# Performance work log

Hardware: AMD Instinct MI355X
Metric: run time of the kernel (lower is better)

## Reference

```python
import jax, jax.numpy as jnp
import numpy as np

N_NODES = 100000
N_EDGES = 600000
IN_DIM = 128
OUT_DIM = 64


def setup_inputs() -> dict:
    key = jax.random.key(0)
    k1, k2, k3, k4, k5 = jax.random.split(key, 5)
    x = jax.random.normal(k1, (N_NODES, IN_DIM), dtype=jnp.float32)
    edge_index = jax.random.randint(k2, (2, N_EDGES), 0, N_NODES, dtype=jnp.int64)
    edge_weight = jax.random.uniform(k3, (N_EDGES,), dtype=jnp.float32)
    W1 = jax.random.normal(k4, (IN_DIM, IN_DIM), dtype=jnp.float32) / np.sqrt(IN_DIM)
    b1 = jnp.zeros((IN_DIM,), dtype=jnp.float32)
    W2 = jax.random.normal(k5, (IN_DIM, OUT_DIM), dtype=jnp.float32) / np.sqrt(IN_DIM)
    b2 = jnp.zeros((OUT_DIM,), dtype=jnp.float32)
    return {"x": x, "edge_index": edge_index, "edge_weight": edge_weight,
            "W1": W1, "b1": b1, "W2": W2, "b2": b2}


def _spmm(edge_index, edge_weight, h):
    # out[dst] = sum_{e: dst(e)=dst} w_e * h[src(e)]  -- normalized adjacency SpMM
    src, dst = edge_index[0], edge_index[1]
    msg = h[src] * edge_weight[:, None]          # [E, D] gather + scale
    return jax.ops.segment_sum(msg, dst, num_segments=h.shape[0])  # [N, D]


def reference(x, edge_index, edge_weight, W1, b1, W2, b2):
    # Layer 1: GCNConv(in,in) -> ReLU (dropout is identity in eval mode)
    h = _spmm(edge_index, edge_weight, x @ W1) + b1
    h = jax.nn.relu(h)
    # Layer 2: GCNConv(in,out)
    out = _spmm(edge_index, edge_weight, h @ W2) + b2
    return out
```

## Files before the change

kernel.cpp:

```cpp
#include <hip/hip_runtime.h>

#define NN 100000
#define NE 600000
#define DIN 128
#define DOUT 64
#define SCAN_B 512
#define NBLK ((NN + SCAN_B - 1) / SCAN_B)
#define HIST_B ((NE + 255) / 256)
#define G1_BM 128
#define G1B ((NN + G1_BM - 1) / G1_BM)
#define GMB ((NN + 63) / 64)
#define ZB ((NN + 255) / 256)
#define W1B (DIN * DIN / 256)
#define W2B (DIN * DOUT / 256)
#define XS_PITCH 136

typedef __attribute__((ext_vector_type(8))) short bf16x8;
typedef __attribute__((ext_vector_type(4))) short s16x4;
typedef __attribute__((ext_vector_type(4))) float f32x4;
typedef __attribute__((ext_vector_type(2))) float f32x2;

__device__ inline short f2bf(float f) {
  union { float f; unsigned u; } v; v.f = f;
  unsigned r = (v.u + 0x7FFF + ((v.u >> 16) & 1)) >> 16;
  return (short)r;
}
__device__ inline float bf2f(unsigned short u) {
  union { unsigned u; float f; } v; v.u = ((unsigned)u) << 16;
  return v.f;
}
__device__ inline unsigned char f2fp8(float f) {
  unsigned pk = __builtin_amdgcn_cvt_pk_fp8_f32(f, f, 0, false);
  return (unsigned char)(pk & 0xff);
}
__device__ inline void fma_fp8x16(uint4 q, float w, float* acc) {
  f32x2 f;
  f = __builtin_amdgcn_cvt_pk_f32_fp8(q.x, false); acc[0] += w * f[0];  acc[1] += w * f[1];
  f = __builtin_amdgcn_cvt_pk_f32_fp8(q.x, true);  acc[2] += w * f[0];  acc[3] += w * f[1];
  f = __builtin_amdgcn_cvt_pk_f32_fp8(q.y, false); acc[4] += w * f[0];  acc[5] += w * f[1];
  f = __builtin_amdgcn_cvt_pk_f32_fp8(q.y, true);  acc[6] += w * f[0];  acc[7] += w * f[1];
  f = __builtin_amdgcn_cvt_pk_f32_fp8(q.z, false); acc[8] += w * f[0];  acc[9] += w * f[1];
  f = __builtin_amdgcn_cvt_pk_f32_fp8(q.z, true);  acc[10] += w * f[0]; acc[11] += w * f[1];
  f = __builtin_amdgcn_cvt_pk_f32_fp8(q.w, false); acc[12] += w * f[0]; acc[13] += w * f[1];
  f = __builtin_amdgcn_cvt_pk_f32_fp8(q.w, true);  acc[14] += w * f[0]; acc[15] += w * f[1];
}

__global__ __launch_bounds__(256) void prep_kernel(int* __restrict__ cnt,
                                                   const float* __restrict__ W1,
                                                   short* __restrict__ w1t,
                                                   const float* __restrict__ W2,
                                                   short* __restrict__ w2t) {
  const int b = blockIdx.x, t = threadIdx.x;
  if (b < ZB) {
    int i = b * 256 + t;
    if (i < NN) cnt[i] = 0;
  } else if (b < ZB + W1B) {
    int i = (b - ZB) * 256 + t;
    int n = i >> 7, k = i & 127;
    w1t[i] = f2bf(W1[k * DIN + n]);
  } else {
    int i = (b - ZB - W1B) * 256 + t;
    int n = i >> 7, k = i & 127;
    w2t[i] = f2bf(W2[k * DOUT + n]);
  }
}

__global__ __launch_bounds__(256) void hist_kernel(const int* __restrict__ ei,
                                                   int* __restrict__ cnt,
                                                   int* __restrict__ rank) {
  int e = blockIdx.x * 256 + threadIdx.x;
  if (e < NE) rank[e] = atomicAdd(&cnt[ei[NE + e]], 1);
}

__global__ __launch_bounds__(512) void scan_local_kernel(const int* __restrict__ cnt,
                                                         int* __restrict__ row_ptr,
                                                         int* __restrict__ blk_sum) {
  __shared__ int s[512];
  const int b = blockIdx.x, t = threadIdx.x;
  const int i = b * 512 + t;
  int v = (i < NN) ? cnt[i] : 0;
  s[t] = v;
  __syncthreads();
  for (int off = 1; off < 512; off <<= 1) {
    int u = (t >= off) ? s[t - off] : 0;
    __syncthreads();
    s[t] += u;
    __syncthreads();
  }
  if (i < NN) row_ptr[i] = s[t] - v;
  if (t == 511) blk_sum[b] = s[511];
}

__global__ __launch_bounds__(512) void scan_add_kernel(int* __restrict__ row_ptr,
                                                       const int* __restrict__ blk_sum) {
  __shared__ int s[512];
  const int b = blockIdx.x, t = threadIdx.x;
  s[t] = (t < NBLK) ? blk_sum[t] : 0;
  __syncthreads();
  for (int off = 1; off < 512; off <<= 1) {
    int u = (t >= off) ? s[t - off] : 0;
    __syncthreads();
    s[t] += u;
    __syncthreads();
  }
  int off = (b > 0) ? s[b - 1] : 0;
  const int i = b * 512 + t;
  if (i < NN) row_ptr[i] += off;
  if (b == 0 && t == 0) row_ptr[NN] = NE;
}

__global__ __launch_bounds__(256) void scatter_kernel(const int* __restrict__ ei,
                                                      const float* __restrict__ ew,
                                                      const int* __restrict__ row_ptr,
                                                      const int* __restrict__ rank,
                                                      int2* __restrict__ ep) {
  int e = blockIdx.x * 256 + threadIdx.x;
  if (e >= NE) return;
  int src = ei[e];
  int dst = ei[NE + e];
  int pos = row_ptr[dst] + rank[e];
  ep[pos] = make_int2(src, __float_as_int(ew[e]));
}

__global__ __launch_bounds__(256) void gemm1_kernel(const float* __restrict__ x,
                                                    const short* __restrict__ w1t,
                                                    unsigned char* __restrict__ h0) {
  __shared__ short xs[64][XS_PITCH];
  const int t = threadIdx.x;
  const int row0 = blockIdx.x * 64;
#pragma unroll
  for (int i = 0; i < 8; ++i) {
    int f = t + i * 256;
    int r = f >> 5, c4 = f & 31;
    int gr = row0 + r;
    float4 v = (gr < NN) ? *(const float4*)&x[(size_t)gr * DIN + c4 * 4]
                         : make_float4(0.f, 0.f, 0.f, 0.f);
    s16x4 s;
    s.x = f2bf(v.x); s.y = f2bf(v.y); s.z = f2bf(v.z); s.w = f2bf(v.w);
    *(s16x4*)&xs[r][c4 * 4] = s;
  }
  __syncthreads();

  const int wave = t >> 6, lane = t & 63;
  const int nlane = lane & 15, quad = lane >> 4;
  const int mbase = wave * 16;
  f32x4 acc[8];
#pragma unroll
  for (int nt = 0; nt < 8; ++nt) acc[nt] = (f32x4){0.f, 0.f, 0.f, 0.f};

#pragma unroll
  for (int ks = 0; ks < 4; ++ks) {
    const int koff = ks * 32 + quad * 8;
    bf16x8 a = *(const bf16x8*)&xs[mbase + nlane][koff];
#pragma unroll
    for (int nt = 0; nt < 8; ++nt) {
      bf16x8 bfr = *(const bf16x8*)&w1t[(size_t)(nt * 16 + nlane) * DIN + koff];
      acc[nt] = __builtin_amdgcn_mfma_f32_16x16x32_bf16(a, bfr, acc[nt], 0, 0, 0);
    }
  }
#pragma unroll
  for (int nt = 0; nt < 8; ++nt)
#pragma unroll
    for (int rg = 0; rg < 4; ++rg) {
      int gr = row0 + mbase + quad * 4 + rg;
      if (gr < NN) h0[(size_t)gr * DIN + nt * 16 + nlane] = f2fp8(acc[nt][rg]);
    }
}

__global__ __launch_bounds__(512) void spmm1_gemm2_kernel(const int* __restrict__ rp,
                                                          const int2* __restrict__ ep,
                                                          const unsigned char* __restrict__ h,
                                                          const float* __restrict__ b1,
                                                          const short* __restrict__ w2t,
                                                          short* __restrict__ h2) {
  __shared__ short xs[G1_BM][XS_PITCH];
  const int t = threadIdx.x;
  const int row0 = blockIdx.x * G1_BM;
  const int sub = t >> 3, lane8 = t & 7;
  float bb[16];
  *(float4*)&bb[0]  = *(const float4*)&b1[lane8 * 16];
  *(float4*)&bb[4]  = *(const float4*)&b1[lane8 * 16 + 4];
  *(float4*)&bb[8]  = *(const float4*)&b1[lane8 * 16 + 8];
  *(float4*)&bb[12] = *(const float4*)&b1[lane8 * 16 + 12];

#pragma unroll
  for (int batch = 0; batch < 2; ++batch) {
    const int r = batch * 64 + sub;
    const int row = row0 + r;
    float acc[16];
#pragma unroll
    for (int j = 0; j < 16; ++j) acc[j] = 0.f;
    if (row < NN) {
      const int b0 = rp[row], e1 = rp[row + 1];
      int i = b0;
      for (; i + 4 <= e1; i += 4) {
        int2 p0 = ep[i], p1 = ep[i + 1], p2 = ep[i + 2], p3 = ep[i + 3];
        uint4 q0 = *(const uint4*)&h[(size_t)p0.x * DIN + lane8 * 16];
        uint4 q1 = *(const uint4*)&h[(size_t)p1.x * DIN + lane8 * 16];
        uint4 q2 = *(const uint4*)&h[(size_t)p2.x * DIN + lane8 * 16];
        uint4 q3 = *(const uint4*)&h[(size_t)p3.x * DIN + lane8 * 16];
        fma_fp8x16(q0, __int_as_float(p0.y), acc);
        fma_fp8x16(q1, __int_as_float(p1.y), acc);
        fma_fp8x16(q2, __int_as_float(p2.y), acc);
        fma_fp8x16(q3, __int_as_float(p3.y), acc);
      }
      if (i + 2 <= e1) {
        int2 p0 = ep[i], p1 = ep[i + 1];
        uint4 q0 = *(const uint4*)&h[(size_t)p0.x * DIN + lane8 * 16];
        uint4 q1 = *(const uint4*)&h[(size_t)p1.x * DIN + lane8 * 16];
        fma_fp8x16(q0, __int_as_float(p0.y), acc);
        fma_fp8x16(q1, __int_as_float(p1.y), acc);
        i += 2;
      }
      if (i < e1) {
        int2 p0 = ep[i];
        uint4 q0 = *(const uint4*)&h[(size_t)p0.x * DIN + lane8 * 16];
        fma_fp8x16(q0, __int_as_float(p0.y), acc);
      }
    }
    bf16x8 o0, o1;
#pragma unroll
    for (int j = 0; j < 8; ++j) {
      o0[j] = f2bf(fmaxf(acc[j] + bb[j], 0.f));
      o1[j] = f2bf(fmaxf(acc[8 + j] + bb[8 + j], 0.f));
    }
    *(bf16x8*)&xs[r][lane8 * 16] = o0;
    *(bf16x8*)&xs[r][lane8 * 16 + 8] = o1;
  }
  __syncthreads();

  const int wave = t >> 6, lane = t & 63;
  const int nlane = lane & 15, quad = lane >> 4;
  const int mbase = wave * 16;
  f32x4 acc2[4];
#pragma unroll
  for (int nt = 0; nt < 4; ++nt) acc2[nt] = (f32x4){0.f, 0.f, 0.f, 0.f};
#pragma unroll
  for (int ks = 0; ks < 4; ++ks) {
    const int koff = ks * 32 + quad * 8;
    bf16x8 a0 = *(const bf16x8*)&xs[mbase + nlane][koff];
#pragma unroll
    for (int nt = 0; nt < 4; ++nt) {
      bf16x8 bfr = *(const bf16x8*)&w2t[(size_t)(nt * 16 + nlane) * DIN + koff];
      acc2[nt] = __builtin_amdgcn_mfma_f32_16x16x32_bf16(a0, bfr, acc2[nt], 0, 0, 0);
    }
  }
#pragma unroll
  for (int nt = 0; nt < 4; ++nt)
#pragma unroll
    for (int rg = 0; rg < 4; ++rg) {
      int gr = row0 + mbase + quad * 4 + rg;
      if (gr < NN) h2[(size_t)gr * DOUT + nt * 16 + nlane] = f2bf(acc2[nt][rg]);
    }
}

__global__ __launch_bounds__(256) void spmm2_kernel(const int* __restrict__ rp,
                                                    const int2* __restrict__ ep,
                                                    const short* __restrict__ h,
                                                    const float* __restrict__ bias,
                                                    float* __restrict__ out) {
  const int row = blockIdx.x * 32 + (threadIdx.x >> 3);
  const int lane = threadIdx.x & 7;
  if (row >= NN) return;
  const int b = rp[row], e = rp[row + 1];
  float acc[8];
#pragma unroll
  for (int j = 0; j < 8; ++j) acc[j] = 0.f;
  int i = b;
  for (; i + 4 <= e; i += 4) {
    int2 p0 = ep[i], p1 = ep[i + 1], p2 = ep[i + 2], p3 = ep[i + 3];
    bf16x8 v0 = *(const bf16x8*)&h[(size_t)p0.x * DOUT + lane * 8];
    bf16x8 v1 = *(const bf16x8*)&h[(size_t)p1.x * DOUT + lane * 8];
    bf16x8 v2 = *(const bf16x8*)&h[(size_t)p2.x * DOUT + lane * 8];
    bf16x8 v3 = *(const bf16x8*)&h[(size_t)p3.x * DOUT + lane * 8];
    float w0 = __int_as_float(p0.y), w1 = __int_as_float(p1.y);
    float w2 = __int_as_float(p2.y), w3 = __int_as_float(p3.y);
#pragma unroll
    for (int j = 0; j < 8; ++j)
      acc[j] += w0 * bf2f((unsigned short)v0[j]) + w1 * bf2f((unsigned short)v1[j]) +
                w2 * bf2f((unsigned short)v2[j]) + w3 * bf2f((unsigned short)v3[j]);
  }
  if (i + 2 <= e) {
    int2 p0 = ep[i], p1 = ep[i + 1];
    bf16x8 v0 = *(const bf16x8*)&h[(size_t)p0.x * DOUT + lane * 8];
    bf16x8 v1 = *(const bf16x8*)&h[(size_t)p1.x * DOUT + lane * 8];
    float w0 = __int_as_float(p0.y), w1 = __int_as_float(p1.y);
#pragma unroll
    for (int j = 0; j < 8; ++j)
      acc[j] += w0 * bf2f((unsigned short)v0[j]) + w1 * bf2f((unsigned short)v1[j]);
    i += 2;
  }
  if (i < e) {
    int2 p0 = ep[i];
    bf16x8 v0 = *(const bf16x8*)&h[(size_t)p0.x * DOUT + lane * 8];
    float w0 = __int_as_float(p0.y);
#pragma unroll
    for (int j = 0; j < 8; ++j) acc[j] += w0 * bf2f((unsigned short)v0[j]);
  }
#pragma unroll
  for (int j = 0; j < 8; ++j) acc[j] += bias[lane * 8 + j];
  *(float4*)&out[(size_t)row * DOUT + lane * 8] = make_float4(acc[0], acc[1], acc[2], acc[3]);
  *(float4*)&out[(size_t)row * DOUT + lane * 8 + 4] = make_float4(acc[4], acc[5], acc[6], acc[7]);
}

extern "C" void kernel_launch(void* const* d_in, const int* in_sizes, int n_in,
                              void* d_out, int out_size, void* d_ws, size_t ws_size,
                              hipStream_t stream) {
  const float* x  = (const float*)d_in[0];
  const int*   ei = (const int*)d_in[1];
  const float* ew = (const float*)d_in[2];
  const float* W1 = (const float*)d_in[3];
  const float* b1 = (const float*)d_in[4];
  const float* W2 = (const float*)d_in[5];
  const float* b2 = (const float*)d_in[6];
  float* out = (float*)d_out;

  char* p = (char*)d_ws;
  int*   cnt     = (int*)p;                 p += sizeof(int) * NN;
  int*   row_ptr = (int*)p;                 p += sizeof(int) * (NN + 4);
  int*   blk_sum = (int*)p;                 p += sizeof(int) * (NBLK + 4);
  int*   rank    = (int*)p;                 p += sizeof(int) * NE;
  int2*  ep      = (int2*)p;                p += sizeof(int2) * NE;
  short* w1t     = (short*)p;               p += sizeof(short) * DIN * DIN;
  short* w2t     = (short*)p;               p += sizeof(short) * DIN * DOUT;
  unsigned char* h0 = (unsigned char*)p;    p += (size_t)NN * DIN;
  short* h2      = (short*)p;

  prep_kernel<<<ZB + W1B + W2B, 256, 0, stream>>>(cnt, W1, w1t, W2, w2t);
  hist_kernel<<<HIST_B, 256, 0, stream>>>(ei, cnt, rank);
  scan_local_kernel<<<NBLK, 512, 0, stream>>>(cnt, row_ptr, blk_sum);
  scan_add_kernel<<<NBLK, 512, 0, stream>>>(row_ptr, blk_sum);
  scatter_kernel<<<HIST_B, 256, 0, stream>>>(ei, ew, row_ptr, rank, ep);
  gemm1_kernel<<<GMB, 256, 0, stream>>>(x, w1t, h0);
  spmm1_gemm2_kernel<<<G1B, 512, 0, stream>>>(row_ptr, ep, h0, b1, w2t, h2);
  spmm2_kernel<<<(NN + 31) / 32, 256, 0, stream>>>(row_ptr, ep, h2, b2, out);
}
```

Measured before the change: 242.6 us.

## Stage GEMM outputs through LDS for coalesced stores; double gemm1 row tile

gemm1 now processes 128 rows per block, so each wave computes two 16-row MFMA tiles that share each W1 fragment load. In both gemm1 and the fused spmm1/gemm2 kernel, the MFMA results are first written into shared memory with a padded pitch and then copied out as 16-byte vector stores per row. This replaces scattered single-byte and two-byte global stores. The cost is extra barriers, more LDS traffic, and higher register use in gemm1.

```diff
diff --git a/kernel.cpp b/kernel.cpp
--- a/kernel.cpp
+++ b/kernel.cpp
@@ -9,11 +9,11 @@
 #define HIST_B ((NE + 255) / 256)
 #define G1_BM 128
 #define G1B ((NN + G1_BM - 1) / G1_BM)
-#define GMB ((NN + 63) / 64)
 #define ZB ((NN + 255) / 256)
 #define W1B (DIN * DIN / 256)
 #define W2B (DIN * DOUT / 256)
 #define XS_PITCH 136
+#define RP_PITCH 144
 
 typedef __attribute__((ext_vector_type(8))) short bf16x8;
 typedef __attribute__((ext_vector_type(4))) short s16x4;
@@ -125,11 +125,11 @@
 __global__ __launch_bounds__(256) void gemm1_kernel(const float* __restrict__ x,
                                                     const short* __restrict__ w1t,
                                                     unsigned char* __restrict__ h0) {
-  __shared__ short xs[64][XS_PITCH];
+  __shared__ short xs[G1_BM][XS_PITCH];
   const int t = threadIdx.x;
-  const int row0 = blockIdx.x * 64;
-#pragma unroll
-  for (int i = 0; i < 8; ++i) {
+  const int row0 = blockIdx.x * G1_BM;
+#pragma unroll
+  for (int i = 0; i < 16; ++i) {
     int f = t + i * 256;
     int r = f >> 5, c4 = f & 31;
     int gr = row0 + r;
@@ -143,28 +143,46 @@
 
   const int wave = t >> 6, lane = t & 63;
   const int nlane = lane & 15, quad = lane >> 4;
-  const int mbase = wave * 16;
-  f32x4 acc[8];
-#pragma unroll
-  for (int nt = 0; nt < 8; ++nt) acc[nt] = (f32x4){0.f, 0.f, 0.f, 0.f};
+  const int mbase = wave * 32;
+  f32x4 acc[2][8];
+#pragma unroll
+  for (int mt = 0; mt < 2; ++mt)
+#pragma unroll
+    for (int nt = 0; nt < 8; ++nt) acc[mt][nt] = (f32x4){0.f, 0.f, 0.f, 0.f};
 
 #pragma unroll
   for (int ks = 0; ks < 4; ++ks) {
     const int koff = ks * 32 + quad * 8;
-    bf16x8 a = *(const bf16x8*)&xs[mbase + nlane][koff];
+    bf16x8 a0 = *(const bf16x8*)&xs[mbase + nlane][koff];
+    bf16x8 a1 = *(const bf16x8*)&xs[mbase + 16 + nlane][koff];
 #pragma unroll
     for (int nt = 0; nt < 8; ++nt) {
-      bf16x8 bfr = *(const bf16x8*)&w1t[(size_t)(nt * 16 + nlane) * DIN + koff];
-      acc[nt] = __builtin_amdgcn_mfma_f32_16x16x32_bf16(a, bfr, acc[nt], 0, 0, 0);
-    }
-  }
-#pragma unroll
-  for (int nt = 0; nt < 8; ++nt)
-#pragma unroll
-    for (int rg = 0; rg < 4; ++rg) {
-      int gr = row0 + mbase + quad * 4 + rg;
-      if (gr < NN) h0[(size_t)gr * DIN + nt * 16 + nlane] = f2fp8(acc[nt][rg]);
-    }
+      bf16x8 b = *(const bf16x8*)&w1t[(size_t)(nt * 16 + nlane) * DIN + koff];
+      acc[0][nt] = __builtin_amdgcn_mfma_f32_16x16x32_bf16(a0, b, acc[0][nt], 0, 0, 0);
+      acc[1][nt] = __builtin_amdgcn_mfma_f32_16x16x32_bf16(a1, b, acc[1][nt], 0, 0, 0);
+    }
+  }
+
+  __syncthreads();
+  unsigned char* lsb = (unsigned char*)xs;
+#pragma unroll
+  for (int mt = 0; mt < 2; ++mt)
+#pragma unroll
+    for (int nt = 0; nt < 8; ++nt)
+#pragma unroll
+      for (int rg = 0; rg < 4; ++rg)
+        lsb[(mbase + mt * 16 + quad * 4 + rg) * RP_PITCH + nt * 16 + nlane] =
+            f2fp8(acc[mt][nt][rg]);
+  __syncthreads();
+  {
+    const int r = t >> 1, half = t & 1;
+    const int gr = row0 + r;
+    if (gr < NN) {
+      const uint4* s = (const uint4*)(lsb + r * RP_PITCH + half * 64);
+      uint4* d = (uint4*)&h0[(size_t)gr * DIN + half * 64];
+      d[0] = s[0]; d[1] = s[1]; d[2] = s[2]; d[3] = s[3];
+    }
+  }
 }
 
 __global__ __launch_bounds__(512) void spmm1_gemm2_kernel(const int* __restrict__ rp,
@@ -245,13 +263,25 @@
       acc2[nt] = __builtin_amdgcn_mfma_f32_16x16x32_bf16(a0, bfr, acc2[nt], 0, 0, 0);
     }
   }
+
+  __syncthreads();
+  unsigned char* lsb = (unsigned char*)xs;
 #pragma unroll
   for (int nt = 0; nt < 4; ++nt)
 #pragma unroll
-    for (int rg = 0; rg < 4; ++rg) {
-      int gr = row0 + mbase + quad * 4 + rg;
-      if (gr < NN) h2[(size_t)gr * DOUT + nt * 16 + nlane] = f2bf(acc2[nt][rg]);
-    }
+    for (int rg = 0; rg < 4; ++rg)
+      *(short*)(lsb + (mbase + quad * 4 + rg) * RP_PITCH + (nt * 16 + nlane) * 2) =
+          f2bf(acc2[nt][rg]);
+  __syncthreads();
+  {
+    const int r = t >> 2, q = t & 3;
+    const int gr = row0 + r;
+    if (gr < NN) {
+      const uint4* s = (const uint4*)(lsb + r * RP_PITCH + q * 32);
+      uint4* d = (uint4*)&h2[(size_t)gr * DOUT + q * 16];
+      d[0] = s[0]; d[1] = s[1];
+    }
+  }
 }
 
 __global__ __launch_bounds__(256) void spmm2_kernel(const int* __restrict__ rp,
@@ -331,7 +361,7 @@
   scan_local_kernel<<<NBLK, 512, 0, stream>>>(cnt, row_ptr, blk_sum);
   scan_add_kernel<<<NBLK, 512, 0, stream>>>(row_ptr, blk_sum);
   scatter_kernel<<<HIST_B, 256, 0, stream>>>(ei, ew, row_ptr, rank, ep);
-  gemm1_kernel<<<GMB, 256, 0, stream>>>(x, w1t, h0);
+  gemm1_kernel<<<G1B, 256, 0, stream>>>(x, w1t, h0);
   spmm1_gemm2_kernel<<<G1B, 512, 0, stream>>>(row_ptr, ep, h0, b1, w2t, h2);
   spmm2_kernel<<<(NN + 31) / 32, 256, 0, stream>>>(row_ptr, ep, h2, b2, out);
 }
```

Result: faster. 231.5 us (-4.6%).
